# Kernel optimization log

Hardware: AMD Instinct MI355X
Metric: run time of the kernel (lower is better)

The kernel has to match this reference:

```python
import jax, jax.numpy as jnp
import numpy as np

EMBED_DIM = 512
NUM_HEADS = 8
WINDOW = 128
B, S = 4, 2048


def setup_inputs() -> dict:
    key = jax.random.key(0)
    k0, k1, k2, k3, k4 = jax.random.split(key, 5)
    scale = 1.0 / np.sqrt(EMBED_DIM)
    return {
        "embeddings": jax.random.normal(k0, (B, S, EMBED_DIM), dtype=jnp.float32),
        "in_proj_w": jax.random.normal(k1, (3 * EMBED_DIM, EMBED_DIM), dtype=jnp.float32) * scale,
        "in_proj_b": jax.random.normal(k2, (3 * EMBED_DIM,), dtype=jnp.float32) * 0.01,
        "out_w": jax.random.normal(k3, (EMBED_DIM, EMBED_DIM), dtype=jnp.float32) * scale,
        "out_b": jax.random.normal(k4, (EMBED_DIM,), dtype=jnp.float32) * 0.01,
    }


def reference(embeddings, in_proj_w, in_proj_b, out_w, out_b):
    b, s, e = embeddings.shape
    h = NUM_HEADS
    dh = e // h
    # combined QKV projection (matches torch nn.MultiheadAttention in_proj)
    qkv = embeddings @ in_proj_w.T + in_proj_b          # [b,s,3e]
    q, k, v = jnp.split(qkv, 3, axis=-1)
    q = q.reshape(b, s, h, dh)
    k = k.reshape(b, s, h, dh)
    v = v.reshape(b, s, h, dh)
    scores = jnp.einsum("bihd,bjhd->bhij", q, k) / jnp.sqrt(jnp.float32(dh))
    # banded window mask: position i attends to [i-W, i+W]
    idx = jnp.arange(s)
    band = jnp.abs(idx[:, None] - idx[None, :]) <= WINDOW   # [s,s] bool
    scores = jnp.where(band, scores, -jnp.inf)
    attn = jax.nn.softmax(scores, axis=-1)                   # [b,h,s,s]
    ctx = jnp.einsum("bhij,bjhd->bihd", attn, v).reshape(b, s, e)
    out = ctx @ out_w.T + out_b                              # [b,s,e]
    pooled = jnp.max(out, axis=1)                            # [b,e]
    weights = jnp.mean(attn, axis=1)                         # head-averaged [b,s,s]
    return pooled, weights
```

## Files before the change

kernel.cpp:

```cpp
#include <hip/hip_runtime.h>
#include <math.h>

#define BB   4
#define SS   2048
#define EE   512
#define HH   8
#define DH   64
#define WW   128
#define MM   (BB*SS)
#define NTILE (SS/32)
#define SWH  296
#define VTP  296
#define BK   64
#define PBH  ((size_t)NTILE*32*288)

typedef _Float16 f16x8 __attribute__((ext_vector_type(8)));
typedef _Float16 f16x2 __attribute__((ext_vector_type(2)));
typedef float    f32x4 __attribute__((ext_vector_type(4)));
typedef unsigned int u32x4 __attribute__((ext_vector_type(4)));

#define GLOAD16(gp, lp) __builtin_amdgcn_global_load_lds( \
    (const __attribute__((address_space(1))) void*)(gp),  \
    (__attribute__((address_space(3))) void*)(lp), 16, 0, 0)

__global__ __launch_bounds__(256) void convert3(
    const float* __restrict__ a, const float* __restrict__ bsrc,
    const float* __restrict__ c,
    _Float16* __restrict__ da, _Float16* __restrict__ db, _Float16* __restrict__ dc)
{
    const size_t na4 = (size_t)MM*EE/4;
    const size_t nb4 = (size_t)3*EE*EE/4;
    const size_t nc4 = (size_t)EE*EE/4;
    const size_t tot = na4 + nb4 + nc4;
    for (size_t i = (size_t)blockIdx.x*256 + threadIdx.x; i < tot;
         i += (size_t)gridDim.x*256) {
        const float* s; _Float16* d; size_t off;
        if (i < na4)            { s = a;    d = da; off = i; }
        else if (i < na4 + nb4) { s = bsrc; d = db; off = i - na4; }
        else                    { s = c;    d = dc; off = i - na4 - nb4; }
        float4 v = ((const float4*)s)[off];
        union { _Float16 h[4]; uint2 u; } o;
        o.h[0] = (_Float16)v.x; o.h[1] = (_Float16)v.y;
        o.h[2] = (_Float16)v.z; o.h[3] = (_Float16)v.w;
        ((uint2*)d)[off] = o.u;
    }
}

__global__ __launch_bounds__(256) void qkv_mfma(
    const _Float16* __restrict__ A, const _Float16* __restrict__ Wt,
    const float* __restrict__ bias,
    _Float16* __restrict__ qd, _Float16* __restrict__ kd, _Float16* __restrict__ vtg)
{
    __shared__ _Float16 As[128*BK];
    __shared__ _Float16 Bs[128*BK];

    const int tid = threadIdx.x;
    const int wid = tid >> 6, lane = tid & 63;
    const int l15 = lane & 15, g = lane >> 4;
    const int wr = wid >> 1, wc = wid & 1;
    const int m0 = blockIdx.x * 128;
    const int n0 = blockIdx.y * 128;

    const int lrow = lane >> 3;
    const int swz  = (lane & 7) ^ lrow;
    const _Float16* Ab = A  + (size_t)(m0 + wid*32 + lrow)*512 + swz*8;
    const _Float16* Bb = Wt + (size_t)(n0 + wid*32 + lrow)*512 + swz*8;

    f32x4 acc[4][4] = {};
    for (int k0 = 0; k0 < 512; k0 += BK) {
        __syncthreads();
        #pragma unroll
        for (int t = 0; t < 4; ++t) {
            GLOAD16(Ab + (size_t)t*8*512 + k0, &As[(wid*32 + t*8)*BK]);
            GLOAD16(Bb + (size_t)t*8*512 + k0, &Bs[(wid*32 + t*8)*BK]);
        }
        __syncthreads();

        f16x8 af[2][4], bf[2][4];
        #pragma unroll
        for (int ks = 0; ks < 2; ++ks)
            #pragma unroll
            for (int f = 0; f < 4; ++f) {
                const int ch = ((ks*4 + g) ^ (l15 & 7)) * 8;
                af[ks][f] = *(const f16x8*)&As[(wr*64 + f*16 + l15)*BK + ch];
                bf[ks][f] = *(const f16x8*)&Bs[(wc*64 + f*16 + l15)*BK + ch];
            }
        #pragma unroll
        for (int ks = 0; ks < 2; ++ks)
            #pragma unroll
            for (int fi = 0; fi < 4; ++fi)
                #pragma unroll
                for (int fj = 0; fj < 4; ++fj)
                    acc[fi][fj] = __builtin_amdgcn_mfma_f32_16x16x32_f16(
                        af[ks][fi], bf[ks][fj], acc[fi][fj], 0, 0, 0);
    }

    const int which = n0 >> 9;
    if (which < 2) {
        _Float16* dst = (which == 0) ? qd : kd;
        #pragma unroll
        for (int fj = 0; fj < 4; ++fj) {
            const int col = n0 + wc*64 + fj*16 + l15;
            const int h = (col >> 6) & 7;
            const float bc = bias[col];
            #pragma unroll
            for (int fi = 0; fi < 4; ++fi)
                #pragma unroll
                for (int rr = 0; rr < 4; ++rr) {
                    int grow = m0 + wr*64 + fi*16 + g*4 + rr;
                    int b = grow >> 11, s = grow & 2047;
                    dst[(((size_t)(b*HH + h))*SS + s)*DH + (col & 63)] =
                        (_Float16)(acc[fi][fj][rr] + bc);
                }
        }
    } else {
        #pragma unroll
        for (int fj = 0; fj < 4; ++fj) {
            const int col = n0 + wc*64 + fj*16 + l15;
            const int h = (col >> 6) & 7;
            const int d = col & 63;
            const float bc = bias[col];
            #pragma unroll
            for (int fi = 0; fi < 4; ++fi) {
                int grow0 = m0 + wr*64 + fi*16 + g*4;
                int b = grow0 >> 11, s0 = grow0 & 2047;
                union { _Float16 h4[4]; uint2 u; } o;
                #pragma unroll
                for (int rr = 0; rr < 4; ++rr)
                    o.h4[rr] = (_Float16)(acc[fi][fj][rr] + bc);
                *(uint2*)(vtg + (((size_t)(b*HH + h))*DH + d)*SS + s0) = o.u;
            }
        }
    }
}

__global__ __launch_bounds__(256) void out_mfma(
    const _Float16* __restrict__ A, const _Float16* __restrict__ Wt,
    const float* __restrict__ bias, float* __restrict__ part)
{
    __shared__ _Float16 As[128*BK];
    __shared__ _Float16 Bs[128*BK];

    const int tid = threadIdx.x;
    const int wid = tid >> 6, lane = tid & 63;
    const int l15 = lane & 15, g = lane >> 4;
    const int wr = wid >> 1, wc = wid & 1;
    const int m0 = blockIdx.x * 128;
    const int n0 = blockIdx.y * 128;

    const int lrow = lane >> 3;
    const int swz  = (lane & 7) ^ lrow;
    const _Float16* Ab = A  + (size_t)(m0 + wid*32 + lrow)*512 + swz*8;
    const _Float16* Bb = Wt + (size_t)(n0 + wid*32 + lrow)*512 + swz*8;

    f32x4 acc[4][4] = {};
    for (int k0 = 0; k0 < 512; k0 += BK) {
        __syncthreads();
        #pragma unroll
        for (int t = 0; t < 4; ++t) {
            GLOAD16(Ab + (size_t)t*8*512 + k0, &As[(wid*32 + t*8)*BK]);
            GLOAD16(Bb + (size_t)t*8*512 + k0, &Bs[(wid*32 + t*8)*BK]);
        }
        __syncthreads();

        f16x8 af[2][4], bf[2][4];
        #pragma unroll
        for (int ks = 0; ks < 2; ++ks)
            #pragma unroll
            for (int f = 0; f < 4; ++f) {
                const int ch = ((ks*4 + g) ^ (l15 & 7)) * 8;
                af[ks][f] = *(const f16x8*)&As[(wr*64 + f*16 + l15)*BK + ch];
                bf[ks][f] = *(const f16x8*)&Bs[(wc*64 + f*16 + l15)*BK + ch];
            }
        #pragma unroll
        for (int ks = 0; ks < 2; ++ks)
            #pragma unroll
            for (int fi = 0; fi < 4; ++fi)
                #pragma unroll
                for (int fj = 0; fj < 4; ++fj)
                    acc[fi][fj] = __builtin_amdgcn_mfma_f32_16x16x32_f16(
                        af[ks][fi], bf[ks][fj], acc[fi][fj], 0, 0, 0);
    }

    __syncthreads();
    float* red = (float*)As;
    #pragma unroll
    for (int fj = 0; fj < 4; ++fj) {
        float cm = -1e30f;
        #pragma unroll
        for (int fi = 0; fi < 4; ++fi)
            #pragma unroll
            for (int rr = 0; rr < 4; ++rr)
                cm = fmaxf(cm, acc[fi][fj][rr]);
        cm = fmaxf(cm, __shfl_xor(cm, 16));
        cm = fmaxf(cm, __shfl_xor(cm, 32));
        if (g == 0) red[wr*128 + wc*64 + fj*16 + l15] = cm;
    }
    __syncthreads();
    if (tid < 128) {
        float m = fmaxf(red[tid], red[128 + tid]) + bias[n0 + tid];
        part[(size_t)blockIdx.x * EE + n0 + tid] = m;
    }
}

__global__ __launch_bounds__(512, 4) void attn_mfma(
    const _Float16* __restrict__ qd, const _Float16* __restrict__ kd,
    const _Float16* __restrict__ vtg, _Float16* __restrict__ ctx,
    unsigned char* __restrict__ pb)
{
    __shared__ _Float16 sc[32 * SWH];
    __shared__ _Float16 vt[64 * VTP];

    const int tid  = threadIdx.x;
    const int wid  = tid >> 6;
    const int lane = tid & 63;
    const int l15  = lane & 15;
    const int g    = lane >> 4;

    const int lin = blockIdx.x + (blockIdx.y << 6) + (blockIdx.z << 8);
    const int nid = (lin & 7) * 256 + (lin >> 3);
    const int ti = nid & 63;
    const int b  = (nid >> 6) & 3;
    const int h  = nid >> 8;

    const int i0 = ti * 32;
    const int jlo = (i0 - WW > 0) ? i0 - WW : 0;
    const int jhi = (i0 + 31 + WW < SS - 1) ? i0 + 31 + WW : SS - 1;
    const int nj = jhi - jlo + 1;
    const int NC = nj >> 4;

    const _Float16* qb = qd  + ((size_t)(b*HH + h))*SS*DH;
    const _Float16* kb = kd  + ((size_t)(b*HH + h))*SS*DH;
    const _Float16* vb = vtg + ((size_t)(b*HH + h))*DH*SS + jlo;

    #pragma unroll
    for (int it = 0; it < 5; ++it) {
        int idx = tid + it*512;
        if (idx < 64*37) {
            int r = idx / 37;
            int c = idx - r*37;
            int csrc = (c < 36) ? c : 35;
            GLOAD16(vb + (size_t)r*SS + csrc*8, &vt[idx*8]);
        }
    }

    if (nj < 288) {
        int row = tid >> 4, pt = tid & 15;
        for (int jj = nj + pt; jj < 288; jj += 16)
            sc[row*SWH + jj] = (_Float16)(-60000.f);
    }

    {
        const int rh = wid & 1, cgrp = wid >> 1;
        const int qrow = i0 + rh*16 + l15;
        f16x8 aq0 = *(const f16x8*)(qb + (size_t)qrow*DH +      g*8);
        f16x8 aq1 = *(const f16x8*)(qb + (size_t)qrow*DH + 32 + g*8);
        #pragma unroll
        for (int t = 0; t < 5; ++t) {
            int c = cgrp + t*4;
            if (c < NC) {
                int jj = c*16 + l15;
                int j  = jlo + jj;
                f16x8 bk0 = *(const f16x8*)(kb + (size_t)j*DH +      g*8);
                f16x8 bk1 = *(const f16x8*)(kb + (size_t)j*DH + 32 + g*8);
                f32x4 s = {0.f, 0.f, 0.f, 0.f};
                s = __builtin_amdgcn_mfma_f32_16x16x32_f16(aq0, bk0, s, 0, 0, 0);
                s = __builtin_amdgcn_mfma_f32_16x16x32_f16(aq1, bk1, s, 0, 0, 0);
                #pragma unroll
                for (int r = 0; r < 4; ++r) {
                    int srow = rh*16 + g*4 + r;
                    int i = i0 + srow;
                    int dd = i - j; if (dd < 0) dd = -dd;
                    float val = (dd <= WW) ? s[r]*0.125f : -60000.f;
                    sc[srow*SWH + jj] = (_Float16)val;
                }
            }
        }
    }
    __syncthreads();

    {
        const int qi = tid >> 4, pt = tid & 15;
        _Float16* srow = &sc[qi*SWH];
        f16x8 v0 = *(const f16x8*)&srow[pt*16];
        f16x8 v1 = *(const f16x8*)&srow[pt*16 + 8];
        f16x2 v2 = *(const f16x2*)&srow[256 + pt*2];
        float x[18];
        #pragma unroll
        for (int e = 0; e < 8; ++e) { x[e] = (float)v0[e]; x[8+e] = (float)v1[e]; }
        x[16] = (float)v2[0]; x[17] = (float)v2[1];

        float mrow = x[0];
        #pragma unroll
        for (int e = 1; e < 18; ++e) mrow = fmaxf(mrow, x[e]);
        #pragma unroll
        for (int o = 1; o < 16; o <<= 1) mrow = fmaxf(mrow, __shfl_xor(mrow, o));

        float ssum = 0.f;
        #pragma unroll
        for (int e = 0; e < 18; ++e) { x[e] = __expf(x[e] - mrow); ssum += x[e]; }
        #pragma unroll
        for (int o = 1; o < 16; o <<= 1) ssum += __shfl_xor(ssum, o);
        const float inv = 1.0f / ssum;

        f16x8 p0, p1;
        f16x2 p2;
        #pragma unroll
        for (int e = 0; e < 8; ++e) {
            p0[e] = (_Float16)(x[e]   * inv);
            p1[e] = (_Float16)(x[8+e] * inv);
        }
        p2[0] = (_Float16)(x[16] * inv);
        p2[1] = (_Float16)(x[17] * inv);
        *(f16x8*)&srow[pt*16]      = p0;
        *(f16x8*)&srow[pt*16 + 8]  = p1;
        *(f16x2*)&srow[256 + pt*2] = p2;

        unsigned char* prow = pb + ((((size_t)(b*HH + h))*NTILE + ti)*32 + qi)*288;
        u32x4 pw;
        #pragma unroll
        for (int q4 = 0; q4 < 4; ++q4) {
            unsigned int w = 0;
            #pragma unroll
            for (int e = 0; e < 4; ++e) {
                unsigned int v = (unsigned int)(x[q4*4 + e] * inv * 255.f + 0.5f);
                w |= v << (8*e);
            }
            pw[q4] = w;
        }
        *(u32x4*)(prow + pt*16) = pw;
        unsigned int t16 = (unsigned int)(x[16] * inv * 255.f + 0.5f);
        unsigned int t17 = (unsigned int)(x[17] * inv * 255.f + 0.5f);
        *(unsigned short*)(prow + 256 + pt*2) = (unsigned short)(t16 | (t17 << 8));
    }
    __syncthreads();

    {
        const int rh = wid & 1, dt = wid >> 1;
        const int d = dt*16 + l15;
        f32x4 acc = {0.f, 0.f, 0.f, 0.f};
        #pragma unroll
        for (int ks = 0; ks < 9; ++ks) {
            f16x8 ap = *(const f16x8*)&sc[(rh*16 + l15)*SWH + ks*32 + g*8];
            f16x8 bv = *(const f16x8*)&vt[(size_t)d*VTP + ks*32 + g*8];
            acc = __builtin_amdgcn_mfma_f32_16x16x32_f16(ap, bv, acc, 0, 0, 0);
        }
        #pragma unroll
        for (int r = 0; r < 4; ++r) {
            int row = i0 + rh*16 + g*4 + r;
            ctx[((size_t)(b*SS + row))*EE + h*DH + d] = (_Float16)acc[r];
        }
    }
}

__global__ __launch_bounds__(256) void reduce_w(
    const unsigned char* __restrict__ pb, float* __restrict__ wout)
{
    const int lin = blockIdx.x + (blockIdx.y << 6) + (blockIdx.z << 8);
    const int W  = (lin & 7) * 128 + (lin >> 3);
    const int tb = W >> 2;
    const int z  = W & 3;
    const int ti = tb & 63;
    const int b  = tb >> 6;

    const int i0 = ti * 32;
    const int jlo = (i0 - WW > 0) ? i0 - WW : 0;

    const int row = threadIdx.x >> 3;
    const int pt  = threadIdx.x & 7;
    const unsigned char* base =
        pb + (((size_t)b*HH*NTILE + ti)*32 + row)*288;
    float* wrow = wout + ((size_t)(b*SS + i0 + row))*SS;
    const float scale = 0.125f / 255.f;

    const int q0 = z * 512;
    for (int j4 = q0 + pt*4; j4 < q0 + 512; j4 += 32) {
        int r4 = j4 - jlo;
        f32x4 o = {0.f, 0.f, 0.f, 0.f};
        if (r4 >= 0 && r4 < 288) {
            float s0 = 0.f, s1 = 0.f, s2 = 0.f, s3 = 0.f;
            #pragma unroll
            for (int h = 0; h < HH; ++h) {
                unsigned int u = *(const unsigned int*)(base + (size_t)h*PBH + r4);
                s0 += (float)(u & 255u);
                s1 += (float)((u >> 8) & 255u);
                s2 += (float)((u >> 16) & 255u);
                s3 += (float)(u >> 24);
            }
            o[0] = s0*scale; o[1] = s1*scale; o[2] = s2*scale; o[3] = s3*scale;
        }
        __builtin_nontemporal_store(o, (f32x4*)(wrow + j4));
    }
}

__global__ void pool_final(const float* __restrict__ part, float* __restrict__ pooled)
{
    int e = blockIdx.x * 256 + threadIdx.x;
    int b = blockIdx.y;
    float m = -1e30f;
    #pragma unroll
    for (int t = 0; t < 16; ++t)
        m = fmaxf(m, part[((size_t)(b*16 + t))*EE + e]);
    pooled[b*EE + e] = m;
}

extern "C" void kernel_launch(void* const* d_in, const int* in_sizes, int n_in,
                              void* d_out, int out_size, void* d_ws, size_t ws_size,
                              hipStream_t stream)
{
    const float* emb = (const float*)d_in[0];
    const float* ipw = (const float*)d_in[1];
    const float* ipb = (const float*)d_in[2];
    const float* ow  = (const float*)d_in[3];
    const float* ob  = (const float*)d_in[4];

    float* pooled = (float*)d_out;
    float* wout   = pooled + (size_t)BB*EE;

    const size_t headsz = (size_t)BB*HH*SS*DH;
    _Float16* q    = (_Float16*)d_ws;
    _Float16* k    = q + headsz;
    _Float16* vtg  = k + headsz;
    _Float16* ctx  = vtg + headsz + 256;
    _Float16* A16  = ctx + (size_t)MM*EE;
    _Float16* W16  = A16 + (size_t)MM*EE;
    _Float16* OW16 = W16 + (size_t)3*EE*EE;
    float* part    = (float*)(OW16 + (size_t)EE*EE);
    unsigned char* pbuf = (unsigned char*)(part + 64*EE);

    convert3<<<1280, 256, 0, stream>>>(emb, ipw, ow, A16, W16, OW16);
    qkv_mfma<<<dim3(64, 12), 256, 0, stream>>>(A16, W16, ipb, q, k, vtg);
    attn_mfma<<<dim3(NTILE, BB, HH), 512, 0, stream>>>(q, k, vtg, ctx, pbuf);
    reduce_w<<<dim3(NTILE, BB, 4), 256, 0, stream>>>(pbuf, wout);
    out_mfma<<<dim3(64, 4), 256, 0, stream>>>(ctx, OW16, ob, part);
    pool_final<<<dim3(2, BB), 256, 0, stream>>>(part, pooled);
}
```

Measured before the change: 95.39 us.

## Add MFMA priority hints, nontemporal prob stores, wider reduce_w loads

Wraps the QK and PV MFMA sequences in s_setprio raises so matrix waves get issue priority. The quantized probability buffer writes become nontemporal stores. reduce_w now handles 8 columns per thread with 8-byte loads and two 16-byte stores instead of 4 columns. The aim is fewer memory instructions and less cache pollution in the bandwidth-bound weight-averaging kernel. Risk: the nontemporal writes may lose L2 reuse when reduce_w reads the buffer back soon after.

```diff
diff --git a/kernel.cpp b/kernel.cpp
--- a/kernel.cpp
+++ b/kernel.cpp
@@ -264,8 +264,10 @@
                 f16x8 bk0 = *(const f16x8*)(kb + (size_t)j*DH +      g*8);
                 f16x8 bk1 = *(const f16x8*)(kb + (size_t)j*DH + 32 + g*8);
                 f32x4 s = {0.f, 0.f, 0.f, 0.f};
+                __builtin_amdgcn_s_setprio(1);
                 s = __builtin_amdgcn_mfma_f32_16x16x32_f16(aq0, bk0, s, 0, 0, 0);
                 s = __builtin_amdgcn_mfma_f32_16x16x32_f16(aq1, bk1, s, 0, 0, 0);
+                __builtin_amdgcn_s_setprio(0);
                 #pragma unroll
                 for (int r = 0; r < 4; ++r) {
                     int srow = rh*16 + g*4 + r;
@@ -328,10 +330,11 @@
             }
             pw[q4] = w;
         }
-        *(u32x4*)(prow + pt*16) = pw;
+        __builtin_nontemporal_store(pw, (u32x4*)(prow + pt*16));
         unsigned int t16 = (unsigned int)(x[16] * inv * 255.f + 0.5f);
         unsigned int t17 = (unsigned int)(x[17] * inv * 255.f + 0.5f);
-        *(unsigned short*)(prow + 256 + pt*2) = (unsigned short)(t16 | (t17 << 8));
+        __builtin_nontemporal_store((unsigned short)(t16 | (t17 << 8)),
+                                    (unsigned short*)(prow + 256 + pt*2));
     }
     __syncthreads();
 
@@ -339,12 +342,14 @@
         const int rh = wid & 1, dt = wid >> 1;
         const int d = dt*16 + l15;
         f32x4 acc = {0.f, 0.f, 0.f, 0.f};
+        __builtin_amdgcn_s_setprio(1);
         #pragma unroll
         for (int ks = 0; ks < 9; ++ks) {
             f16x8 ap = *(const f16x8*)&sc[(rh*16 + l15)*SWH + ks*32 + g*8];
             f16x8 bv = *(const f16x8*)&vt[(size_t)d*VTP + ks*32 + g*8];
             acc = __builtin_amdgcn_mfma_f32_16x16x32_f16(ap, bv, acc, 0, 0, 0);
         }
+        __builtin_amdgcn_s_setprio(0);
         #pragma unroll
         for (int r = 0; r < 4; ++r) {
             int row = i0 + rh*16 + g*4 + r;
@@ -374,22 +379,26 @@
     const float scale = 0.125f / 255.f;
 
     const int q0 = z * 512;
-    for (int j4 = q0 + pt*4; j4 < q0 + 512; j4 += 32) {
-        int r4 = j4 - jlo;
-        f32x4 o = {0.f, 0.f, 0.f, 0.f};
-        if (r4 >= 0 && r4 < 288) {
-            float s0 = 0.f, s1 = 0.f, s2 = 0.f, s3 = 0.f;
+    for (int j8 = q0 + pt*8; j8 < q0 + 512; j8 += 64) {
+        int r8 = j8 - jlo;
+        f32x4 o0 = {0.f, 0.f, 0.f, 0.f};
+        f32x4 o1 = {0.f, 0.f, 0.f, 0.f};
+        if (r8 >= 0 && r8 < 288) {
+            float s[8] = {};
             #pragma unroll
             for (int h = 0; h < HH; ++h) {
-                unsigned int u = *(const unsigned int*)(base + (size_t)h*PBH + r4);
-                s0 += (float)(u & 255u);
-                s1 += (float)((u >> 8) & 255u);
-                s2 += (float)((u >> 16) & 255u);
-                s3 += (float)(u >> 24);
-            }
-            o[0] = s0*scale; o[1] = s1*scale; o[2] = s2*scale; o[3] = s3*scale;
-        }
-        __builtin_nontemporal_store(o, (f32x4*)(wrow + j4));
+                uint2 u = *(const uint2*)(base + (size_t)h*PBH + r8);
+                #pragma unroll
+                for (int e = 0; e < 4; ++e) {
+                    s[e]     += (float)((u.x >> (8*e)) & 255u);
+                    s[4 + e] += (float)((u.y >> (8*e)) & 255u);
+                }
+            }
+            #pragma unroll
+            for (int e = 0; e < 4; ++e) { o0[e] = s[e]*scale; o1[e] = s[4+e]*scale; }
+        }
+        __builtin_nontemporal_store(o0, (f32x4*)(wrow + j8));
+        __builtin_nontemporal_store(o1, (f32x4*)(wrow + j8 + 4));
     }
 }
 
```

New measurement: 109.9 us. 15.2% more time.
